# Kernel optimization log

Hardware: AMD Instinct MI355X
Metric: run time of the kernel (lower is better)

## Reference

```python
import jax, jax.numpy as jnp
import numpy as np

GAMMA = 0.5

def setup_inputs() -> dict:
    key = jax.random.key(0)
    k1, k2 = jax.random.split(key)
    x = jax.random.normal(k1, (4096, 256), dtype=jnp.float32)
    W = jax.random.normal(k2, (256, 512), dtype=jnp.float32)
    return {"x": x, "W": W}

def reference(x, W):
    # difference: (B, D, N) = (B, D, 1) - (D, N)
    diff = x[:, :, None] - W[None, :, :]
    sq_dist = jnp.sum(diff * diff, axis=1)          # (B, N)
    return jnp.exp(-GAMMA * sq_dist)                # (B, N)
```

## Files before the change

kernel.cpp:

```cpp
#include <hip/hip_runtime.h>


#define GAMMA 0.5f
#define B_  4096
#define D_  256
#define N_  512
#define BM  64
#define BN  64
#define LDT 264

typedef __attribute__((ext_vector_type(8))) short bf16x8;
typedef __attribute__((ext_vector_type(4))) float f32x4;
typedef __attribute__((ext_vector_type(4))) float float4v;

__device__ __forceinline__ unsigned short f2bf(float f) {
    union { float f; unsigned int i; } u; u.f = f;
    return (unsigned short)(u.i >> 16);
}

__global__ __launch_bounds__(256, 2)
void rbf_kernel(const float* __restrict__ x, const float* __restrict__ W,
                float* __restrict__ out) {
    __shared__ unsigned short xs[BM][LDT];
    __shared__ float x2s[BM];

    const int tid = threadIdx.x;

    const int bid = blockIdx.x;
    const int wgid = (bid & 7) * 64 + (bid >> 3);
    const int bx = wgid & 7;
    const int by = wgid >> 3;

    {
        const int row = tid >> 2, q = tid & 3;
        const float* xp = x + (size_t)(by * BM + row) * D_ + q * 64;
        unsigned short* lp = &xs[row][q * 64];
        float s = 0.f;
        #pragma unroll
        for (int c = 0; c < 8; ++c) {
            float4v v0 = *(const float4v*)(xp + c * 8);
            float4v v1 = *(const float4v*)(xp + c * 8 + 4);
            s += v0.x*v0.x + v0.y*v0.y + v0.z*v0.z + v0.w*v0.w
               + v1.x*v1.x + v1.y*v1.y + v1.z*v1.z + v1.w*v1.w;
            bf16x8 o = { (short)f2bf(v0.x), (short)f2bf(v0.y), (short)f2bf(v0.z), (short)f2bf(v0.w),
                         (short)f2bf(v1.x), (short)f2bf(v1.y), (short)f2bf(v1.z), (short)f2bf(v1.w) };
            *(bf16x8*)(lp + c * 8) = o;
        }
        s += __shfl_xor(s, 1);
        s += __shfl_xor(s, 2);
        if (q == 0) x2s[row] = s;
    }
    __syncthreads();

    const int l = tid & 63, w = tid >> 6;
    const int wr = w >> 1, wc = w & 1;
    const int lr = l & 15, g = l >> 4;

    const float* Wg = W + bx * BN + wc * 32 + lr;
    float w2p0 = 0.f, w2p1 = 0.f;
    f32x4 acc[2][2] = {{{0,0,0,0},{0,0,0,0}},{{0,0,0,0},{0,0,0,0}}};

    #pragma unroll
    for (int kk = 0; kk < 8; ++kk) {
        const int k0 = kk * 32 + g * 8;
        const float* wp = Wg + (size_t)k0 * N_;
        float w0[8], w1[8];
        #pragma unroll
        for (int j = 0; j < 8; ++j) {
            w0[j] = wp[(size_t)j * N_];
            w1[j] = wp[(size_t)j * N_ + 16];
        }
        bf16x8 b0, b1;
        #pragma unroll
        for (int j = 0; j < 8; ++j) {
            b0[j] = (short)f2bf(w0[j]); b1[j] = (short)f2bf(w1[j]);
            w2p0 += w0[j] * w0[j];      w2p1 += w1[j] * w1[j];
        }
        bf16x8 a0 = *(const bf16x8*)&xs[wr * 32 + lr][k0];
        bf16x8 a1 = *(const bf16x8*)&xs[wr * 32 + 16 + lr][k0];
        acc[0][0] = __builtin_amdgcn_mfma_f32_16x16x32_bf16(a0, b0, acc[0][0], 0, 0, 0);
        acc[0][1] = __builtin_amdgcn_mfma_f32_16x16x32_bf16(a0, b1, acc[0][1], 0, 0, 0);
        acc[1][0] = __builtin_amdgcn_mfma_f32_16x16x32_bf16(a1, b0, acc[1][0], 0, 0, 0);
        acc[1][1] = __builtin_amdgcn_mfma_f32_16x16x32_bf16(a1, b1, acc[1][1], 0, 0, 0);
    }

    w2p0 += __shfl_xor(w2p0, 16); w2p0 += __shfl_xor(w2p0, 32);
    w2p1 += __shfl_xor(w2p1, 16); w2p1 += __shfl_xor(w2p1, 32);

    const float c2l = -(GAMMA) * 1.4426950408889634f;
    float* outp = out + (size_t)(by * BM) * N_ + bx * BN;
    #pragma unroll
    for (int m = 0; m < 2; ++m) {
        #pragma unroll
        for (int n = 0; n < 2; ++n) {
            const int ac = wc * 32 + n * 16 + lr;
            const float w2v = n ? w2p1 : w2p0;
            #pragma unroll
            for (int i = 0; i < 4; ++i) {
                const int ar = wr * 32 + m * 16 + g * 4 + i;
                const float s = x2s[ar] + w2v - 2.f * acc[m][n][i];
                outp[(size_t)ar * N_ + ac] = exp2f(s * c2l);
            }
        }
    }
}

extern "C" void kernel_launch(void* const* d_in, const int* in_sizes, int n_in,
                              void* d_out, int out_size, void* d_ws, size_t ws_size,
                              hipStream_t stream) {
    const float* x = (const float*)d_in[0];
    const float* W = (const float*)d_in[1];
    float* out = (float*)d_out;
    rbf_kernel<<<dim3(512), dim3(256), 0, stream>>>(x, W, out);
}
```

Measured before the change: 64.08 us.

## Double block size to 512 threads, each wave computing a 32x16 output slice

Workgroups grow from 4 to 8 waves. Each wave now computes a 32x16 sub-tile with two MFMAs per k-step instead of a 32x32 sub-tile with four. The x staging is spread over 8 threads per row, with an extra shuffle for the row norm. This is meant to add more latency-hiding parallelism for the strided W global loads and cut per-thread register use. In exchange, each block loads more redundant x A-fragments from LDS, and per-wave MFMA reuse is lower.

New measurement: 64.90 us. Within noise of the previous version (+1.3%).

```diff
diff --git a/kernel.cpp b/kernel.cpp
--- a/kernel.cpp
+++ b/kernel.cpp
@@ -18,7 +18,7 @@
     return (unsigned short)(u.i >> 16);
 }
 
-__global__ __launch_bounds__(256, 2)
+__global__ __launch_bounds__(512, 4)
 void rbf_kernel(const float* __restrict__ x, const float* __restrict__ W,
                 float* __restrict__ out) {
     __shared__ unsigned short xs[BM][LDT];
@@ -32,12 +32,12 @@
     const int by = wgid >> 3;
 
     {
-        const int row = tid >> 2, q = tid & 3;
-        const float* xp = x + (size_t)(by * BM + row) * D_ + q * 64;
-        unsigned short* lp = &xs[row][q * 64];
+        const int row = tid >> 3, q = tid & 7;
+        const float* xp = x + (size_t)(by * BM + row) * D_ + q * 32;
+        unsigned short* lp = &xs[row][q * 32];
         float s = 0.f;
         #pragma unroll
-        for (int c = 0; c < 8; ++c) {
+        for (int c = 0; c < 4; ++c) {
             float4v v0 = *(const float4v*)(xp + c * 8);
             float4v v1 = *(const float4v*)(xp + c * 8 + 4);
             s += v0.x*v0.x + v0.y*v0.y + v0.z*v0.z + v0.w*v0.w
@@ -48,59 +48,52 @@
         }
         s += __shfl_xor(s, 1);
         s += __shfl_xor(s, 2);
+        s += __shfl_xor(s, 4);
         if (q == 0) x2s[row] = s;
     }
     __syncthreads();
 
     const int l = tid & 63, w = tid >> 6;
-    const int wr = w >> 1, wc = w & 1;
+    const int wr = w >> 2, wc = w & 3;
     const int lr = l & 15, g = l >> 4;
 
-    const float* Wg = W + bx * BN + wc * 32 + lr;
-    float w2p0 = 0.f, w2p1 = 0.f;
-    f32x4 acc[2][2] = {{{0,0,0,0},{0,0,0,0}},{{0,0,0,0},{0,0,0,0}}};
+    const float* Wg = W + bx * BN + wc * 16 + lr;
+    float w2p = 0.f;
+    f32x4 acc0 = {0,0,0,0}, acc1 = {0,0,0,0};
 
     #pragma unroll
     for (int kk = 0; kk < 8; ++kk) {
         const int k0 = kk * 32 + g * 8;
         const float* wp = Wg + (size_t)k0 * N_;
-        float w0[8], w1[8];
+        float w0[8];
+        #pragma unroll
+        for (int j = 0; j < 8; ++j) w0[j] = wp[(size_t)j * N_];
+        bf16x8 b0;
         #pragma unroll
         for (int j = 0; j < 8; ++j) {
-            w0[j] = wp[(size_t)j * N_];
-            w1[j] = wp[(size_t)j * N_ + 16];
-        }
-        bf16x8 b0, b1;
-        #pragma unroll
-        for (int j = 0; j < 8; ++j) {
-            b0[j] = (short)f2bf(w0[j]); b1[j] = (short)f2bf(w1[j]);
-            w2p0 += w0[j] * w0[j];      w2p1 += w1[j] * w1[j];
+            b0[j] = (short)f2bf(w0[j]);
+            w2p += w0[j] * w0[j];
         }
         bf16x8 a0 = *(const bf16x8*)&xs[wr * 32 + lr][k0];
         bf16x8 a1 = *(const bf16x8*)&xs[wr * 32 + 16 + lr][k0];
-        acc[0][0] = __builtin_amdgcn_mfma_f32_16x16x32_bf16(a0, b0, acc[0][0], 0, 0, 0);
-        acc[0][1] = __builtin_amdgcn_mfma_f32_16x16x32_bf16(a0, b1, acc[0][1], 0, 0, 0);
-        acc[1][0] = __builtin_amdgcn_mfma_f32_16x16x32_bf16(a1, b0, acc[1][0], 0, 0, 0);
-        acc[1][1] = __builtin_amdgcn_mfma_f32_16x16x32_bf16(a1, b1, acc[1][1], 0, 0, 0);
+        acc0 = __builtin_amdgcn_mfma_f32_16x16x32_bf16(a0, b0, acc0, 0, 0, 0);
+        acc1 = __builtin_amdgcn_mfma_f32_16x16x32_bf16(a1, b0, acc1, 0, 0, 0);
     }
 
-    w2p0 += __shfl_xor(w2p0, 16); w2p0 += __shfl_xor(w2p0, 32);
-    w2p1 += __shfl_xor(w2p1, 16); w2p1 += __shfl_xor(w2p1, 32);
+    w2p += __shfl_xor(w2p, 16);
+    w2p += __shfl_xor(w2p, 32);
 
     const float c2l = -(GAMMA) * 1.4426950408889634f;
     float* outp = out + (size_t)(by * BM) * N_ + bx * BN;
+    const int ac = wc * 16 + lr;
     #pragma unroll
     for (int m = 0; m < 2; ++m) {
+        const f32x4 a = m ? acc1 : acc0;
         #pragma unroll
-        for (int n = 0; n < 2; ++n) {
-            const int ac = wc * 32 + n * 16 + lr;
-            const float w2v = n ? w2p1 : w2p0;
-            #pragma unroll
-            for (int i = 0; i < 4; ++i) {
-                const int ar = wr * 32 + m * 16 + g * 4 + i;
-                const float s = x2s[ar] + w2v - 2.f * acc[m][n][i];
-                outp[(size_t)ar * N_ + ac] = exp2f(s * c2l);
-            }
+        for (int i = 0; i < 4; ++i) {
+            const int ar = wr * 32 + m * 16 + g * 4 + i;
+            const float s = x2s[ar] + w2p - 2.f * a[i];
+            outp[(size_t)ar * N_ + ac] = exp2f(s * c2l);
         }
     }
 }
@@ -111,5 +104,5 @@
     const float* x = (const float*)d_in[0];
     const float* W = (const float*)d_in[1];
     float* out = (float*)d_out;
-    rbf_kernel<<<dim3(512), dim3(256), 0, stream>>>(x, W, out);
+    rbf_kernel<<<dim3(512), dim3(512), 0, stream>>>(x, W, out);
 }
```
